# Optimization experiments

Hardware: AMD Instinct MI355X
Metric: run time of the kernel (lower is better)

Reference implementation:

```python
import jax, jax.numpy as jnp
import numpy as np

FEATURE_SIZES = (5, 5, 3, 8, 6, 2)  # sums to 29
K = 64  # truncation rank (k < min(H, W) -> truncation branch of evaluateSSVD)
B, H, W = 256, 128, 128
A = 128  # action dim (rows of weightsO)


def _conv1d(x, w, b, stride, pad):
    # x: [N, 1, L]; w: [kw]; b: scalar. Degenerate Conv3d(1,1,(1,1,kw)) along last axis.
    y = jax.lax.conv_general_dilated(x, w.reshape(1, 1, -1), (stride,), [(pad, pad)])
    return y + b


def setup_inputs() -> dict:
    key = jax.random.key(0)
    ks = jax.random.split(key, 8)
    obs = jax.random.uniform(ks[0], (B, H, W, 29), dtype=jnp.float32)
    weights1 = jax.random.normal(ks[1], (4, K, K), dtype=jnp.float32) * 0.1
    weights2 = jax.random.normal(ks[2], (4, K, K), dtype=jnp.float32) * 0.1
    weightsO = jax.random.normal(ks[3], (A, H * W), dtype=jnp.float32) * 0.02
    conv1_w = jax.random.normal(ks[4], (4,), dtype=jnp.float32) * 0.5
    conv1_b = jnp.zeros((1,), dtype=jnp.float32)
    conv2_w = jax.random.normal(ks[5], (2,), dtype=jnp.float32) * 0.5
    conv2_b = jnp.zeros((1,), dtype=jnp.float32)
    return {"obs": obs, "weights1": weights1, "weights2": weights2,
            "weightsO": weightsO, "conv1_w": conv1_w, "conv1_b": conv1_b,
            "conv2_w": conv2_w, "conv2_b": conv2_b}


def reference(obs, weights1, weights2, weightsO, conv1_w, conv1_b, conv2_w, conv2_b):
    b, h, w, d = obs.shape
    # --- feature compression: weighted sum of each plane group with arange weights ---
    feats = []
    p = 0
    for size in FEATURE_SIZES:
        wts = jnp.arange(size, dtype=obs.dtype)
        feats.append(jnp.einsum('bhwd,d->bhw', obs[..., p:p + size], wts))
        p += size
    x = jnp.stack(feats, axis=-1)  # [B,H,W,6]
    # --- conv chain along feature axis: 6 -> 4 -> 3 -> 2 -> 1 ---
    x = x.reshape(b * h * w, 1, len(FEATURE_SIZES))
    for _ in range(3):
        x = _conv1d(x, conv1_w, conv1_b[0], stride=2, pad=2)
    x = _conv1d(x, conv2_w, conv2_b[0], stride=1, pad=0)  # [B*H*W,1,1]
    M = x.reshape(b, h, w)  # per-sample matrix fed to SVD

    def eval_one(m):
        # truncated SVD (k < min(H,W) -> truncation branch of original)
        U, S, Vh = jnp.linalg.svd(m, full_matrices=False)
        Sigma = jnp.diag(S[:K])            # [k,k]
        U = U[:, :K]                       # [H,k]
        Vh = Vh[:K, :]                     # [k,W]
        U_st, _ = jnp.linalg.qr(U)         # [H,k]
        Vq, _ = jnp.linalg.qr(Vh.T)        # [W,k]
        Vh_st = Vq.T                       # [k,W]
        r = jax.nn.relu(U_st @ weights1[0])
        for i in range(1, weights1.shape[0]):
            r = jax.nn.relu(r @ weights1[i])
        r = jax.nn.relu(r @ Sigma)
        # NOTE: original loop starts at 1, so weights2[0] is intentionally unused
        for i in range(1, weights2.shape[0]):
            r = jax.nn.relu(r @ weights2[i])
        return weightsO @ (r @ Vh_st).reshape(-1)  # [A]

    return jax.vmap(eval_one)(M)  # [B, A]
```

## Files before the change

### kernel.cpp

```cpp
#include <hip/hip_runtime.h>


#define NSTR 132
#define U32_OFF 0
#define V32_OFF 8448
#define RA_OFF  16896
#define RB_OFF  25344
#define WF_OFF  33792
#define POOL_BYTES 151552

#define WAVE_FENCE() do { __asm__ __volatile__("" ::: "memory"); \
                          __builtin_amdgcn_wave_barrier();        \
                          __asm__ __volatile__("" ::: "memory"); } while (0)

template<int CTRL>
__device__ __forceinline__ double dpp_d(double x) {
    union { double d; int i[2]; } u, r;
    u.d = x;
    r.i[0] = __builtin_amdgcn_update_dpp(0, u.i[0], CTRL, 0xF, 0xF, true);
    r.i[1] = __builtin_amdgcn_update_dpp(0, u.i[1], CTRL, 0xF, 0xF, true);
    return r.d;
}
__device__ __forceinline__ double slot8_sum(double g) {
    g += dpp_d<0xB1>(g);
    g += dpp_d<0x4E>(g);
    g += dpp_d<0x141>(g);
    return g;
}

#define ROT_ANGLE(d_, g_, cc_, ss_) do {                                  \
    float d32 = (float)(d_), g32 = (float)(g_);                           \
    float h32 = sqrtf(fmaf(d32, d32, 4.0f*g32*g32));                      \
    float den = d32 + copysignf(h32, d32);                                \
    float t32 = __fdividef(2.0f*g32, den);                                \
    float c32 = rsqrtf(fmaf(t32, t32, 1.0f));                             \
    cc_ = (double)c32; ss_ = (double)(t32*c32);                           \
    double corr_ = 0.5*(3.0 - fma(cc_,cc_, ss_*ss_));                     \
    cc_ *= corr_; ss_ *= corr_;                                           \
} while (0)

__global__ __launch_bounds__(256) void k_feat(const float* __restrict__ obs,
        const float* __restrict__ c1w, const float* __restrict__ c1b,
        const float* __restrict__ c2w, const float* __restrict__ c2b,
        double* __restrict__ M)
{
    __shared__ __align__(16) float lds[256*29];
    const int t = threadIdx.x;
    const float4* obs4 = (const float4*)obs;
    float4* lds4 = (float4*)lds;
    const size_t base4 = (size_t)blockIdx.x * 1856;
    for (int idx = t; idx < 1856; idx += 256) lds4[idx] = obs4[base4 + idx];
    __syncthreads();
    const float* o = &lds[t*29];
    double f0=0,f1=0,f2=0,f3=0,f4=0,f5=0;
    #pragma unroll
    for (int d=1; d<5; ++d) f0 += (double)o[d]*d;
    #pragma unroll
    for (int d=1; d<5; ++d) f1 += (double)o[5+d]*d;
    f2 = (double)o[11] + 2.0*(double)o[12];
    #pragma unroll
    for (int d=1; d<8; ++d) f3 += (double)o[13+d]*d;
    #pragma unroll
    for (int d=1; d<6; ++d) f4 += (double)o[21+d]*d;
    f5 = (double)o[28];
    const double w0=c1w[0], w1=c1w[1], w2=c1w[2], w3=c1w[3], b1=c1b[0];
    const double cw0=c2w[0], cw1=c2w[1], b2=c2b[0];
    double y0 = b1 + f0*w2 + f1*w3;
    double y1 = b1 + f0*w0 + f1*w1 + f2*w2 + f3*w3;
    double y2 = b1 + f2*w0 + f3*w1 + f4*w2 + f5*w3;
    double y3 = b1 + f4*w0 + f5*w1;
    double z0 = b1 + y0*w2 + y1*w3;
    double z1 = b1 + y0*w0 + y1*w1 + y2*w2 + y3*w3;
    double z2 = b1 + y2*w0 + y3*w1;
    double u0 = b1 + z0*w2 + z1*w3;
    double u1 = b1 + z0*w0 + z1*w1 + z2*w2;
    double m  = b2 + u0*cw0 + u1*cw1;
    M[(size_t)blockIdx.x*256 + t] = m;
}

__global__ __launch_bounds__(512, 2) void k_svd(
        const float* __restrict__ w1g, const float* __restrict__ w2g,
        double* __restrict__ wsM)
{
    __shared__ __align__(16) char smem[POOL_BYTES];
    double* Ad = (double*)smem;
    float*  Af = (float*)smem;
    __shared__ double colnorm[128];
    __shared__ double sig_d[128];
    __shared__ double sigs_d[64];
    __shared__ float  sigf[64];
    __shared__ double tau2[2][64];
    __shared__ double vjs2[2][64];
    __shared__ int    perm[128];
    __shared__ int    redflag[8];
    __shared__ int    convflag;

    const int t = threadIdx.x;
    const int b = blockIdx.x;
    double* Mg = wsM + (size_t)b*16384;

    const int wv   = t >> 6;
    const int lk   = t & 63;
    const int slot = lk >> 3;
    const int sub  = lk & 7;

    for (int idx = t; idx < 16384; idx += 512) {
        int r = idx >> 7, c = idx & 127;
        Ad[c*NSTR + r] = Mg[idx];
    }
    __syncthreads();

    {
        const int gs = t >> 3;
        #pragma unroll
        for (int h = 0; h < 2; ++h) {
            const int c = gs + 64*h;
            const double2* P = (const double2*)&Ad[c*NSTR + 2*sub];
            double sacc = 0.0;
            #pragma unroll
            for (int m = 0; m < 8; ++m) {
                double2 v = P[m*8];
                sacc = fma(v.x, v.x, sacc); sacc = fma(v.y, v.y, sacc);
            }
            sacc = slot8_sum(sacc);
            if (sub == 0) colnorm[c] = sacc;
        }
    }
    __syncthreads();

    for (int sweep = 0; sweep < 16; ++sweep) {
        int big = 0;

        {
            const int ca = 16*wv + slot, cb = ca + 8;
            double2* PA = (double2*)&Ad[ca*NSTR + 2*sub];
            double2* PB = (double2*)&Ad[cb*NSTR + 2*sub];
            double2 a8[8], b8[8];
            #pragma unroll
            for (int m = 0; m < 8; ++m) { a8[m] = PA[m*8]; b8[m] = PB[m*8]; }
            double nA = colnorm[ca], nB = colnorm[cb];
            for (int s = 1; s < 8; ++s) {
                const int pa = 16*wv + (slot ^ s), pb = pa + 8;
                const double2* QA = (const double2*)&Ad[pa*NSTR + 2*sub];
                const double2* QB = (const double2*)&Ad[pb*NSTR + 2*sub];
                double2 ya[8], yb[8];
                #pragma unroll
                for (int m = 0; m < 8; ++m) { ya[m] = QA[m*8]; yb[m] = QB[m*8]; }
                double nya = colnorm[pa], nyb = colnorm[pb];
                double gA0=0.0, gA1=0.0, gB0=0.0, gB1=0.0;
                #pragma unroll
                for (int m = 0; m < 4; ++m) {
                    gA0 = fma(a8[m].x, ya[m].x, gA0); gA0 = fma(a8[m].y, ya[m].y, gA0);
                    gB0 = fma(b8[m].x, yb[m].x, gB0); gB0 = fma(b8[m].y, yb[m].y, gB0);
                }
                #pragma unroll
                for (int m = 4; m < 8; ++m) {
                    gA1 = fma(a8[m].x, ya[m].x, gA1); gA1 = fma(a8[m].y, ya[m].y, gA1);
                    gB1 = fma(b8[m].x, yb[m].x, gB1); gB1 = fma(b8[m].y, yb[m].y, gB1);
                }
                double gA = slot8_sum(gA0 + gA1);
                double gB = slot8_sum(gB0 + gB1);
                const int pside = (slot < (slot ^ s));
                {
                    double al = pside ? nA : nya, be = pside ? nya : nA;
                    double g2 = gA*gA, pr = al*be;
                    big |= (g2 > pr*1e-20);
                    double cc, ss; ROT_ANGLE(be - al, gA, cc, ss);
                    const bool rot = (g2 > pr*1e-28);
                    cc = rot ? cc : 1.0; ss = rot ? ss : 0.0;
                    double sgn = pside ? -ss : ss;
                    #pragma unroll
                    for (int m = 0; m < 8; ++m) {
                        a8[m].x = fma(sgn, ya[m].x, cc*a8[m].x);
                        a8[m].y = fma(sgn, ya[m].y, cc*a8[m].y);
                    }
                    double cs2 = 2.0*cc*ss*gA;
                    nA = pside ? fma(cc*cc, nA, fma(ss*ss, nya, -cs2))
                               : fma(ss*ss, nya, fma(cc*cc, nA,  cs2));
                }
                {
                    double al = pside ? nB : nyb, be = pside ? nyb : nB;
                    double g2 = gB*gB, pr = al*be;
                    big |= (g2 > pr*1e-20);
                    double cc, ss; ROT_ANGLE(be - al, gB, cc, ss);
                    const bool rot = (g2 > pr*1e-28);
                    cc = rot ? cc : 1.0; ss = rot ? ss : 0.0;
                    double sgn = pside ? -ss : ss;
                    #pragma unroll
                    for (int m = 0; m < 8; ++m) {
                        b8[m].x = fma(sgn, yb[m].x, cc*b8[m].x);
                        b8[m].y = fma(sgn, yb[m].y, cc*b8[m].y);
                    }
                    double cs2 = 2.0*cc*ss*gB;
                    nB = pside ? fma(cc*cc, nB, fma(ss*ss, nyb, -cs2))
                               : fma(ss*ss, nyb, fma(cc*cc, nB,  cs2));
                }
                #pragma unroll
                for (int m = 0; m < 8; ++m) { PA[m*8] = a8[m]; PB[m*8] = b8[m]; }
                if (sub == 0) { colnorm[ca] = nA; colnorm[cb] = nB; }
                WAVE_FENCE();
            }
        }
        __syncthreads();

        for (int r = 0; r < 15; ++r) {
            int GI, GJ;
            if (wv == 0) { GI = 15; GJ = r; }
            else { GI = (r + wv) % 15; GJ = (r - wv + 15) % 15; }
            const int pc = GI*8 + slot, qc0 = GJ*8 + slot;
            double2* Pp = (double2*)&Ad[pc*NSTR + 2*sub];
            double2* Pq = (double2*)&Ad[qc0*NSTR + 2*sub];
            double2 p8[8], q8[8];
            #pragma unroll
            for (int m = 0; m < 8; ++m) { p8[m] = Pp[m*8]; q8[m] = Pq[m*8]; }
            double np = colnorm[pc], nq = colnorm[qc0];
            #pragma unroll
            for (int s = 0; s < 8; ++s) {
                double g0 = 0.0, g1 = 0.0;
                #pragma unroll
                for (int m = 0; m < 4; ++m) {
                    g0 = fma(p8[m].x, q8[m].x, g0);
                    g0 = fma(p8[m].y, q8[m].y, g0);
                }
                #pragma unroll
                for (int m = 4; m < 8; ++m) {
                    g1 = fma(p8[m].x, q8[m].x, g1);
                    g1 = fma(p8[m].y, q8[m].y, g1);
                }
                double ga = slot8_sum(g0 + g1);
                double g2 = ga*ga, pr = np*nq;
                big |= (g2 > pr*1e-20);
                double cc, ss; ROT_ANGLE(nq - np, ga, cc, ss);
                const bool rot = (g2 > pr*1e-28);
                cc = rot ? cc : 1.0; ss = rot ? ss : 0.0;
                #pragma unroll
                for (int m = 0; m < 8; ++m) {
                    double ox = p8[m].x, oy = p8[m].y;
                    p8[m].x = fma(-ss, q8[m].x, cc*ox);
                    p8[m].y = fma(-ss, q8[m].y, cc*oy);
                    q8[m].x = fma( ss, ox, cc*q8[m].x);
                    q8[m].y = fma( ss, oy, cc*q8[m].y);
                }
                double cs2 = 2.0*cc*ss*ga;
                double npn = fma(cc*cc, np, fma(ss*ss, nq, -cs2));
                nq         = fma(ss*ss, np, fma(cc*cc, nq,  cs2));
                np = npn;
                if (s < 7) {
                    const int d8 = ((s ^ (s+1)) << 3);
                    if (d8 == 8) {
                        #pragma unroll
                        for (int m = 0; m < 8; ++m) {
                            q8[m].x = dpp_d<0x128>(q8[m].x);
                            q8[m].y = dpp_d<0x128>(q8[m].y);
                        }
                        nq = dpp_d<0x128>(nq);
                    } else {
                        #pragma unroll
                        for (int m = 0; m < 8; ++m) {
                            q8[m].x = __shfl_xor(q8[m].x, d8);
                            q8[m].y = __shfl_xor(q8[m].y, d8);
                        }
                        nq = __shfl_xor(nq, d8);
                    }
                }
            }
            #pragma unroll
            for (int m = 0; m < 8; ++m) Pp[m*8] = p8[m];
            const int qcf = GJ*8 + (slot ^ 7);
            double2* Pqw = (double2*)&Ad[qcf*NSTR + 2*sub];
            #pragma unroll
            for (int m = 0; m < 8; ++m) Pqw[m*8] = q8[m];
            if (sub == 0) { colnorm[pc] = np; colnorm[qcf] = nq; }
            __syncthreads();
        }

        unsigned long long bb = __ballot(big);
        if (lk == 0) redflag[wv] = (bb != 0ULL) ? 1 : 0;
        __syncthreads();
        if (t == 0) {
            int any = 0;
            for (int i = 0; i < 8; ++i) any |= redflag[i];
            convflag = !any;
        }
        __syncthreads();
        if (convflag) break;
    }
    __syncthreads();

    if (t < 128) {
        double s = 0.0;
        for (int r = 0; r < 128; ++r) { double v = Ad[t*NSTR + r]; s = fma(v, v, s); }
        sig_d[t] = sqrt(s);
    }
    __syncthreads();
    if (t < 128) {
        double my = sig_d[t]; int rk = 0;
        for (int c = 0; c < 128; ++c) {
            double v = sig_d[c];
            rk += (v > my) || (v == my && c < t);
        }
        perm[rk] = t;
    }
    __syncthreads();
    if (t < 64) { sigs_d[t] = sig_d[perm[t]]; sigf[t] = (float)sig_d[perm[t]]; }
    __syncthreads();

    {
        double tmp[16];
        #pragma unroll
        for (int i = 0; i < 16; ++i) {
            int idx = t + i*512; int k = idx >> 7, r = idx & 127;
            tmp[i] = Ad[perm[k]*NSTR + r] / sigs_d[k];
        }
        __syncthreads();
        #pragma unroll
        for (int i = 0; i < 16; ++i) {
            int idx = t + i*512; int k = idx >> 7, r = idx & 127;
            Ad[k*NSTR + r] = tmp[i];
        }
    }
    __syncthreads();

    {
        const int j = t & 127, kh = (t >> 7)*16;
        double acc[16];
        #pragma unroll
        for (int m = 0; m < 16; ++m) acc[m] = 0.0;
        for (int r = 0; r < 128; ++r) {
            double mv = Mg[r*128 + j];
            #pragma unroll
            for (int m = 0; m < 16; ++m) acc[m] = fma(mv, Ad[(kh+m)*NSTR + r], acc[m]);
        }
        #pragma unroll
        for (int m = 0; m < 16; ++m) Ad[(64+kh+m)*NSTR + j] = acc[m] / sigs_d[kh+m];
    }
    __syncthreads();

    {
        const int h  = t >> 8;
        const int t5 = t & 255;
        const int CB = h * 64;
        const int g4 = t5 >> 2, s4 = t5 & 3;
        for (int j = 0; j < 64; ++j) {
            if (t5 < 64) {
                double ps = 0.0;
                for (int r = j + t5; r < 128; r += 64) { double v = Ad[(CB+j)*NSTR + r]; ps = fma(v, v, ps); }
                ps += dpp_d<0xB1>(ps);
                ps += dpp_d<0x4E>(ps);
                ps += dpp_d<0x141>(ps);
                ps += dpp_d<0x128>(ps);
                ps += __shfl_xor(ps, 16);
                ps += __shfl_xor(ps, 32);
                if (t5 == 0) {
                    double piv = Ad[(CB+j)*NSTR + j];
                    double nx = sqrt(ps);
                    double vj = piv + ((piv >= 0.0) ? nx : -nx);
                    double vn2 = ps - piv*piv + vj*vj;
                    tau2[h][j] = 2.0 / vn2;
                    vjs2[h][j] = vj;
                    Ad[(CB+j)*NSTR + j] = vj;
                }
            }
            __syncthreads();
            {
                int c = j + 1 + g4;
                if (c < 64) {
                    double w = 0.0;
                    for (int r = j + s4; r < 128; r += 4)
                        w = fma(Ad[(CB+j)*NSTR + r], Ad[(CB+c)*NSTR + r], w);
                    w += dpp_d<0xB1>(w);
                    w += dpp_d<0x4E>(w);
                    w *= tau2[h][j];
                    for (int r = j + s4; r < 128; r += 4)
                        Ad[(CB+c)*NSTR + r] -= w * Ad[(CB+j)*NSTR + r];
                }
            }
            __syncthreads();
        }
        for (int j = 63; j >= 0; --j) {
            {
                int c = j + 1 + g4;
                if (c < 64) {
                    double w = 0.0;
                    for (int r = j + s4; r < 128; r += 4)
                        w = fma(Ad[(CB+j)*NSTR + r], Ad[(CB+c)*NSTR + r], w);
                    w += dpp_d<0xB1>(w);
                    w += dpp_d<0x4E>(w);
                    w *= tau2[h][j];
                    for (int r = j + s4; r < 128; r += 4)
                        Ad[(CB+c)*NSTR + r] -= w * Ad[(CB+j)*NSTR + r];
                }
            }
            __syncthreads();
            if (t5 < 128) {
                double qv;
                if (t5 < j) qv = 0.0;
                else {
                    double vt = Ad[(CB+j)*NSTR + t5];
                    qv = ((t5 == j) ? 1.0 : 0.0) - tau2[h][j]*vjs2[h][j]*vt;
                }
                Ad[(CB+j)*NSTR + t5] = qv;
            }
            __syncthreads();
        }
    }

    {
        float tmpf[16];
        #pragma unroll
        for (int i = 0; i < 16; ++i) {
            int idx = t + i*512; int k = idx >> 7, r = idx & 127;
            tmpf[i] = (float)Ad[k*NSTR + r];
        }
        __syncthreads();
        #pragma unroll
        for (int i = 0; i < 16; ++i) {
            int idx = t + i*512; int k = idx >> 7, r = idx & 127;
            Af[U32_OFF + k*132 + r] = tmpf[i];
        }
        __syncthreads();
        #pragma unroll
        for (int i = 0; i < 16; ++i) {
            int idx = t + i*512; int k = idx >> 7, r = idx & 127;
            tmpf[i] = (float)Ad[(64+k)*NSTR + r];
        }
        __syncthreads();
        #pragma unroll
        for (int i = 0; i < 16; ++i) {
            int idx = t + i*512; int k = idx >> 7, r = idx & 127;
            Af[V32_OFF + k*132 + r] = tmpf[i];
        }
    }
    __syncthreads();

    int SRCO = U32_OFF, DSTO = RA_OFF;
    const int n = t & 63, ib = (t >> 6)*16;
    for (int layer = 0; layer < 7; ++layer) {
        const float* wptr = (layer < 4) ? (w1g + layer*4096) : (w2g + (layer-3)*4096);
        for (int idx = t; idx < 4096; idx += 512) Af[WF_OFF + idx] = wptr[idx];
        __syncthreads();
        float acc[16];
        #pragma unroll
        for (int m = 0; m < 16; ++m) acc[m] = 0.f;
        for (int kk = 0; kk < 64; ++kk) {
            float wv2 = Af[WF_OFF + kk*64 + n];
            const float4* s4v = (const float4*)&Af[SRCO + kk*132 + ib];
            #pragma unroll
            for (int q4 = 0; q4 < 4; ++q4) {
                float4 v4 = s4v[q4];
                acc[q4*4+0] = fmaf(v4.x, wv2, acc[q4*4+0]);
                acc[q4*4+1] = fmaf(v4.y, wv2, acc[q4*4+1]);
                acc[q4*4+2] = fmaf(v4.z, wv2, acc[q4*4+2]);
                acc[q4*4+3] = fmaf(v4.w, wv2, acc[q4*4+3]);
            }
        }
        float sc = (layer == 3) ? sigf[n] : 1.f;
        #pragma unroll
        for (int q4 = 0; q4 < 4; ++q4) {
            float4 o;
            o.x = fmaxf(acc[q4*4+0], 0.f)*sc;
            o.y = fmaxf(acc[q4*4+1], 0.f)*sc;
            o.z = fmaxf(acc[q4*4+2], 0.f)*sc;
            o.w = fmaxf(acc[q4*4+3], 0.f)*sc;
            ((float4*)&Af[DSTO + n*132 + ib])[q4] = o;
        }
        __syncthreads();
        SRCO = DSTO; DSTO = (DSTO == RA_OFF) ? RB_OFF : RA_OFF;
    }

    {
        float* Tb = (float*)((char*)wsM + (size_t)b*131072);
        const int j2 = t & 127, ih = (t >> 7)*32;
        float acc2[32];
        #pragma unroll
        for (int m = 0; m < 32; ++m) acc2[m] = 0.f;
        for (int kk = 0; kk < 64; ++kk) {
            float vv = Af[V32_OFF + kk*132 + j2];
            const float4* r4 = (const float4*)&Af[RA_OFF + kk*132 + ih];
            #pragma unroll
            for (int q4 = 0; q4 < 8; ++q4) {
                float4 v4 = r4[q4];
                acc2[q4*4+0] = fmaf(v4.x, vv, acc2[q4*4+0]);
                acc2[q4*4+1] = fmaf(v4.y, vv, acc2[q4*4+1]);
                acc2[q4*4+2] = fmaf(v4.z, vv, acc2[q4*4+2]);
                acc2[q4*4+3] = fmaf(v4.w, vv, acc2[q4*4+3]);
            }
        }
        #pragma unroll
        for (int m = 0; m < 32; ++m) Tb[(size_t)(ih+m)*128 + j2] = acc2[m];
    }
}

__global__ __launch_bounds__(256) void k_out(const char* __restrict__ wsbase,
        const float* __restrict__ wO, float* __restrict__ part)
{
    __shared__ float Wt[128*65];
    __shared__ float Tt[8*64];
    const int t = threadIdx.x;
    const int bt = blockIdx.x & 31, ks = blockIdx.x >> 5;
    const int a = t & 127, bh = (t >> 7)*4;
    float acc[4] = {0.f, 0.f, 0.f, 0.f};
    for (int cc = 0; cc < 32; ++cc) {
        const int kbase = ks*2048 + cc*64;
        __syncthreads();
        for (int idx = t; idx < 8192; idx += 256) {
            int aa = idx >> 6, nn = idx & 63;
            Wt[aa*65 + nn] = wO[aa*16384 + kbase + nn];
        }
        for (int idx = t; idx < 512; idx += 256) {
            int bl = idx >> 6, nn = idx & 63;
            const float* Tb = (const float*)(wsbase + (size_t)(bt*8 + bl)*131072);
            Tt[bl*64 + nn] = Tb[kbase + nn];
        }
        __syncthreads();
        for (int nn = 0; nn < 64; ++nn) {
            float wv = Wt[a*65 + nn];
            #pragma unroll
            for (int m = 0; m < 4; ++m) acc[m] = fmaf(Tt[(bh+m)*64 + nn], wv, acc[m]);
        }
    }
    #pragma unroll
    for (int m = 0; m < 4; ++m)
        part[ks*32768 + (bt*8 + bh + m)*128 + a] = acc[m];
}

__global__ __launch_bounds__(256) void k_red(const float* __restrict__ part,
                                             float* __restrict__ out)
{
    int i = blockIdx.x*256 + threadIdx.x;
    float s = 0.f;
    #pragma unroll
    for (int ks = 0; ks < 8; ++ks) s += part[ks*32768 + i];
    out[i] = s;
}

extern "C" void kernel_launch(void* const* d_in, const int* in_sizes, int n_in,
                              void* d_out, int out_size, void* d_ws, size_t ws_size,
                              hipStream_t stream)
{
    (void)in_sizes; (void)n_in; (void)out_size; (void)ws_size;
    const float* obs = (const float*)d_in[0];
    const float* w1  = (const float*)d_in[1];
    const float* w2  = (const float*)d_in[2];
    const float* wO  = (const float*)d_in[3];
    const float* c1w = (const float*)d_in[4];
    const float* c1b = (const float*)d_in[5];
    const float* c2w = (const float*)d_in[6];
    const float* c2b = (const float*)d_in[7];
    double* M = (double*)d_ws;
    float* part = (float*)((char*)d_ws + 33554432);

    k_feat<<<dim3(16384), dim3(256), 0, stream>>>(obs, c1w, c1b, c2w, c2b, M);
    k_svd <<<dim3(256),   dim3(512), 0, stream>>>(w1, w2, M);
    k_out <<<dim3(256),   dim3(256), 0, stream>>>((const char*)d_ws, wO, part);
    k_red <<<dim3(128),   dim3(256), 0, stream>>>(part, (float*)d_out);
}
```

Measured before the change: 2.003 ms.

## Presort Jacobi columns by norm and skip rotations no lane needs

Before the one-sided Jacobi sweeps, the columns are ranked by norm, and the matrix and its norms are permuted into descending order. The aim is faster convergence, so fewer sweeps run. Inside both the intra-wave and the tournament rotation phases, the angle computation, the column update and the LDS write-back are now guarded by a wave-wide vote (`__any`) on whether any lane needs a rotation. This skips arithmetic and shared-memory stores in late, nearly converged sweeps. The cost is an extra O(n^2) ranking pass, a full matrix permutation through registers before the sweeps, and extra branches. The column permutation also changes the order of the singular values, which the later code must tolerate.

After: 1.997 ms. About the same (-0.3%).

```diff
diff --git a/kernel.cpp b/kernel.cpp
--- a/kernel.cpp
+++ b/kernel.cpp
@@ -128,6 +128,33 @@
     }
     __syncthreads();
 
+    if (t < 128) {
+        double my = colnorm[t]; int rk = 0;
+        for (int c2 = 0; c2 < 128; ++c2) {
+            double v = colnorm[c2];
+            rk += (v > my) || (v == my && c2 < t);
+        }
+        perm[rk] = t;
+    }
+    __syncthreads();
+    {
+        double tmp[32]; double cn = 0.0;
+        #pragma unroll
+        for (int i = 0; i < 32; ++i) {
+            int idx = t + i*512; int k = idx >> 7, r = idx & 127;
+            tmp[i] = Ad[perm[k]*NSTR + r];
+        }
+        if (t < 128) cn = colnorm[perm[t]];
+        __syncthreads();
+        #pragma unroll
+        for (int i = 0; i < 32; ++i) {
+            int idx = t + i*512; int k = idx >> 7, r = idx & 127;
+            Ad[k*NSTR + r] = tmp[i];
+        }
+        if (t < 128) colnorm[t] = cn;
+    }
+    __syncthreads();
+
     for (int sweep = 0; sweep < 16; ++sweep) {
         int big = 0;
 
@@ -165,39 +192,46 @@
                     double al = pside ? nA : nya, be = pside ? nya : nA;
                     double g2 = gA*gA, pr = al*be;
                     big |= (g2 > pr*1e-20);
-                    double cc, ss; ROT_ANGLE(be - al, gA, cc, ss);
                     const bool rot = (g2 > pr*1e-28);
-                    cc = rot ? cc : 1.0; ss = rot ? ss : 0.0;
-                    double sgn = pside ? -ss : ss;
-                    #pragma unroll
-                    for (int m = 0; m < 8; ++m) {
-                        a8[m].x = fma(sgn, ya[m].x, cc*a8[m].x);
-                        a8[m].y = fma(sgn, ya[m].y, cc*a8[m].y);
+                    if (__any(rot)) {
+                        double cc, ss; ROT_ANGLE(be - al, gA, cc, ss);
+                        cc = rot ? cc : 1.0; ss = rot ? ss : 0.0;
+                        double sgn = pside ? -ss : ss;
+                        #pragma unroll
+                        for (int m = 0; m < 8; ++m) {
+                            a8[m].x = fma(sgn, ya[m].x, cc*a8[m].x);
+                            a8[m].y = fma(sgn, ya[m].y, cc*a8[m].y);
+                        }
+                        double cs2 = 2.0*cc*ss*gA;
+                        nA = pside ? fma(cc*cc, nA, fma(ss*ss, nya, -cs2))
+                                   : fma(ss*ss, nya, fma(cc*cc, nA,  cs2));
+                        #pragma unroll
+                        for (int m = 0; m < 8; ++m) PA[m*8] = a8[m];
+                        if (sub == 0) colnorm[ca] = nA;
                     }
-                    double cs2 = 2.0*cc*ss*gA;
-                    nA = pside ? fma(cc*cc, nA, fma(ss*ss, nya, -cs2))
-                               : fma(ss*ss, nya, fma(cc*cc, nA,  cs2));
                 }
                 {
                     double al = pside ? nB : nyb, be = pside ? nyb : nB;
                     double g2 = gB*gB, pr = al*be;
                     big |= (g2 > pr*1e-20);
-                    double cc, ss; ROT_ANGLE(be - al, gB, cc, ss);
                     const bool rot = (g2 > pr*1e-28);
-                    cc = rot ? cc : 1.0; ss = rot ? ss : 0.0;
-                    double sgn = pside ? -ss : ss;
-                    #pragma unroll
-                    for (int m = 0; m < 8; ++m) {
-                        b8[m].x = fma(sgn, yb[m].x, cc*b8[m].x);
-                        b8[m].y = fma(sgn, yb[m].y, cc*b8[m].y);
+                    if (__any(rot)) {
+                        double cc, ss; ROT_ANGLE(be - al, gB, cc, ss);
+                        cc = rot ? cc : 1.0; ss = rot ? ss : 0.0;
+                        double sgn = pside ? -ss : ss;
+                        #pragma unroll
+                        for (int m = 0; m < 8; ++m) {
+                            b8[m].x = fma(sgn, yb[m].x, cc*b8[m].x);
+                            b8[m].y = fma(sgn, yb[m].y, cc*b8[m].y);
+                        }
+                        double cs2 = 2.0*cc*ss*gB;
+                        nB = pside ? fma(cc*cc, nB, fma(ss*ss, nyb, -cs2))
+                                   : fma(ss*ss, nyb, fma(cc*cc, nB,  cs2));
+                        #pragma unroll
+                        for (int m = 0; m < 8; ++m) PB[m*8] = b8[m];
+                        if (sub == 0) colnorm[cb] = nB;
                     }
-                    double cs2 = 2.0*cc*ss*gB;
-                    nB = pside ? fma(cc*cc, nB, fma(ss*ss, nyb, -cs2))
-                               : fma(ss*ss, nyb, fma(cc*cc, nB,  cs2));
-                }
-                #pragma unroll
-                for (int m = 0; m < 8; ++m) { PA[m*8] = a8[m]; PB[m*8] = b8[m]; }
-                if (sub == 0) { colnorm[ca] = nA; colnorm[cb] = nB; }
+                }
                 WAVE_FENCE();
             }
         }
@@ -214,6 +248,7 @@
             #pragma unroll
             for (int m = 0; m < 8; ++m) { p8[m] = Pp[m*8]; q8[m] = Pq[m*8]; }
             double np = colnorm[pc], nq = colnorm[qc0];
+            bool wrote = false;
             #pragma unroll
             for (int s = 0; s < 8; ++s) {
                 double g0 = 0.0, g1 = 0.0;
@@ -230,21 +265,24 @@
                 double ga = slot8_sum(g0 + g1);
                 double g2 = ga*ga, pr = np*nq;
                 big |= (g2 > pr*1e-20);
-                double cc, ss; ROT_ANGLE(nq - np, ga, cc, ss);
                 const bool rot = (g2 > pr*1e-28);
-                cc = rot ? cc : 1.0; ss = rot ? ss : 0.0;
-                #pragma unroll
-                for (int m = 0; m < 8; ++m) {
-                    double ox = p8[m].x, oy = p8[m].y;
-                    p8[m].x = fma(-ss, q8[m].x, cc*ox);
-                    p8[m].y = fma(-ss, q8[m].y, cc*oy);
-                    q8[m].x = fma( ss, ox, cc*q8[m].x);
-                    q8[m].y = fma( ss, oy, cc*q8[m].y);
-                }
-                double cs2 = 2.0*cc*ss*ga;
-                double npn = fma(cc*cc, np, fma(ss*ss, nq, -cs2));
-                nq         = fma(ss*ss, np, fma(cc*cc, nq,  cs2));
-                np = npn;
+                if (__any(rot)) {
+                    double cc, ss; ROT_ANGLE(nq - np, ga, cc, ss);
+                    cc = rot ? cc : 1.0; ss = rot ? ss : 0.0;
+                    #pragma unroll
+                    for (int m = 0; m < 8; ++m) {
+                        double ox = p8[m].x, oy = p8[m].y;
+                        p8[m].x = fma(-ss, q8[m].x, cc*ox);
+                        p8[m].y = fma(-ss, q8[m].y, cc*oy);
+                        q8[m].x = fma( ss, ox, cc*q8[m].x);
+                        q8[m].y = fma( ss, oy, cc*q8[m].y);
+                    }
+                    double cs2 = 2.0*cc*ss*ga;
+                    double npn = fma(cc*cc, np, fma(ss*ss, nq, -cs2));
+                    nq         = fma(ss*ss, np, fma(cc*cc, nq,  cs2));
+                    np = npn;
+                    wrote = true;
+                }
                 if (s < 7) {
                     const int d8 = ((s ^ (s+1)) << 3);
                     if (d8 == 8) {
@@ -264,13 +302,15 @@
                     }
                 }
             }
-            #pragma unroll
-            for (int m = 0; m < 8; ++m) Pp[m*8] = p8[m];
-            const int qcf = GJ*8 + (slot ^ 7);
-            double2* Pqw = (double2*)&Ad[qcf*NSTR + 2*sub];
-            #pragma unroll
-            for (int m = 0; m < 8; ++m) Pqw[m*8] = q8[m];
-            if (sub == 0) { colnorm[pc] = np; colnorm[qcf] = nq; }
+            if (wrote) {
+                #pragma unroll
+                for (int m = 0; m < 8; ++m) Pp[m*8] = p8[m];
+                const int qcf = GJ*8 + (slot ^ 7);
+                double2* Pqw = (double2*)&Ad[qcf*NSTR + 2*sub];
+                #pragma unroll
+                for (int m = 0; m < 8; ++m) Pqw[m*8] = q8[m];
+                if (sub == 0) { colnorm[pc] = np; colnorm[qcf] = nq; }
+            }
             __syncthreads();
         }
 
```
